# Optimization experiments

Hardware: AMD Instinct MI355X
Metric: run time of the kernel (lower is better)

## Reference

```python
import jax, jax.numpy as jnp
import numpy as np

DIM = 256
B = 8
H = 56
W = 56
K = 2
EPS = 1e-5  # torch BatchNorm2d default eps


def _conv1x1(x, w, b):
    # x: [B,C,H,W], w: [O,C], b: [O]
    return jnp.einsum('oc,bchw->bohw', w, x) + b[None, :, None, None]


def _bn(x, g, be, m, v):
    # inference-mode BatchNorm2d with running stats
    s = g / jnp.sqrt(v + EPS)
    return x * s[None, :, None, None] + (be - m * s)[None, :, None, None]


def _grapher(x, w1, b1, g1, be1, m1, v1, wg, bg, gg, beg, mg, vg, w2, b2, g2, be2, m2, v2):
    # fc1: 1x1 conv + BN
    h = _bn(_conv1x1(x, w1, b1), g1, be1, m1, v1)
    Hh, Ww = h.shape[2], h.shape[3]
    # MRConv4d: running max over circular-shift differences
    # torch.cat([x[:,:,-i:,:], x[:,:,:-i,:]], dim=2) == jnp.roll(x, i, axis=2)
    xj = jnp.zeros_like(h)

    def body_h(c, i):
        return jnp.maximum(c, h - jnp.roll(h, i, axis=2)), None

    xj, _ = jax.lax.scan(body_h, xj, jnp.arange(K, Hh, K))

    def body_w(c, i):
        return jnp.maximum(c, h - jnp.roll(h, i, axis=3)), None

    xj, _ = jax.lax.scan(body_w, xj, jnp.arange(K, Ww, K))

    cat = jnp.concatenate([h, xj], axis=1)  # [B, 2*dim, H, W]
    # MRConv4d.nn: Conv2d(2*dim, 2*dim, 1) -> BN(2*dim) -> GELU (exact erf)
    g = jax.nn.gelu(_bn(_conv1x1(cat, wg, bg), gg, beg, mg, vg), approximate=False)
    # fc2: Conv2d(2*dim, dim, 1) + BN(dim), then residual
    return _bn(_conv1x1(g, w2, b2), g2, be2, m2, v2) + x


def setup_inputs() -> dict:
    key = jax.random.key(0)
    ks = jax.random.split(key, 12)
    d, d2 = DIM, 2 * DIM

    def w(k, o, c):
        return jax.random.normal(k, (o, c), jnp.float32) * np.float32(1.0 / np.sqrt(c))

    return {
        'x': jax.random.normal(ks[0], (B, d, H, W), jnp.float32),
        'w1': w(ks[1], d, d), 'b1': jnp.zeros((d,), jnp.float32),
        'g1': jnp.ones((d,), jnp.float32), 'be1': jnp.zeros((d,), jnp.float32),
        'm1': jax.random.normal(ks[2], (d,), jnp.float32) * 0.1,
        'v1': jax.random.uniform(ks[3], (d,), jnp.float32, 0.5, 1.5),
        'wg': w(ks[4], d2, d2), 'bg': jnp.zeros((d2,), jnp.float32),
        'gg': jnp.ones((d2,), jnp.float32), 'beg': jnp.zeros((d2,), jnp.float32),
        'mg': jax.random.normal(ks[5], (d2,), jnp.float32) * 0.1,
        'vg': jax.random.uniform(ks[6], (d2,), jnp.float32, 0.5, 1.5),
        'w2': w(ks[7], d, d2), 'b2': jnp.zeros((d,), jnp.float32),
        'g2': jnp.ones((d,), jnp.float32), 'be2': jnp.zeros((d,), jnp.float32),
        'm2': jax.random.normal(ks[8], (d,), jnp.float32) * 0.1,
        'v2': jax.random.uniform(ks[9], (d,), jnp.float32, 0.5, 1.5),
    }


def reference(x, w1, b1, g1, be1, m1, v1, wg, bg, gg, beg, mg, vg, w2, b2, g2, be2, m2, v2):
    return _grapher(x, w1, b1, g1, be1, m1, v1, wg, bg, gg, beg, mg, vg, w2, b2, g2, be2, m2, v2)
```

## Files before the change

### kernel.cpp

```cpp
#include <hip/hip_runtime.h>
#include <math.h>

#define SPB 3136
#define NB 8
#define MTOT (NB*SPB)
#define EPS 1e-5f

typedef unsigned short u16;
typedef __attribute__((ext_vector_type(8))) short short8;
typedef __attribute__((ext_vector_type(4))) float float4v;

__device__ __forceinline__ float b2f(u16 v){ unsigned u=((unsigned)v)<<16; float f; __builtin_memcpy(&f,&u,4); return f; }
__device__ __forceinline__ u16 f2b(float f){ unsigned u; __builtin_memcpy(&u,&f,4); u += 0x7fffu + ((u>>16)&1u); return (u16)(u>>16); }
__device__ __forceinline__ float gelu_f(float z){
  float t = 1.5957691216f * z * (1.0f + 0.044715f*z*z);
  return __fdividef(z, 1.0f + __expf(-t));
}

__device__ __forceinline__ void gll16(const u16* g, u16* l){
  __builtin_amdgcn_global_load_lds((const __attribute__((address_space(1))) void*)g,
                                   (__attribute__((address_space(3))) void*)l, 16, 0, 0);
}

__global__ void prep_consts_k(const float* b1,const float* g1,const float* be1,const float* m1,const float* v1,
                              const float* bg,const float* gg,const float* beg,const float* mg,const float* vg,
                              const float* b2,const float* g2,const float* be2,const float* m2,const float* v2,
                              float* cst){
  int i = threadIdx.x;
  if (i < 256) {
    float s = g1[i]*rsqrtf(v1[i]+EPS);
    cst[i] = s; cst[256+i] = b1[i]*s + be1[i] - m1[i]*s;
    float s2 = g2[i]*rsqrtf(v2[i]+EPS);
    cst[1536+i] = s2; cst[1792+i] = b2[i]*s2 + be2[i] - m2[i]*s2;
  }
  float s = gg[i]*rsqrtf(vg[i]+EPS);
  cst[512+i] = s; cst[1024+i] = bg[i]*s + beg[i] - mg[i]*s;
}

__global__ void conv_w_k(const float* __restrict__ w1,const float* __restrict__ wg,const float* __restrict__ w2,
                         u16* __restrict__ w1b,u16* __restrict__ wgb,u16* __restrict__ w2b){
  int i = blockIdx.x*256 + threadIdx.x;
  if (i < 65536)  w1b[i] = f2b(w1[i]);
  if (i < 262144) wgb[i] = f2b(wg[i]);
  if (i < 131072) w2b[i] = f2b(w2[i]);
}

__global__ void transpose_x_k(const float* __restrict__ x, u16* __restrict__ xt){
  __shared__ float t[32][33];
  int b = blockIdx.z, ct = blockIdx.y, st = blockIdx.x;
  int ts = threadIdx.x, tc = threadIdx.y;
  #pragma unroll
  for (int i=0;i<4;i++){
    int c = tc + i*8;
    t[c][ts] = x[((size_t)(b*256 + ct*32 + c))*SPB + st*32 + ts];
  }
  __syncthreads();
  #pragma unroll
  for (int i=0;i<4;i++){
    int r = tc + i*8;
    xt[((size_t)(b*SPB + st*32 + r))*256 + ct*32 + ts] = f2b(t[ts][r]);
  }
}

__global__ void rowmin_k(const u16* __restrict__ cat, float* __restrict__ rmin){
  int b = blockIdx.x/56, y = blockIdx.x%56, c = threadIdx.x;
  float mE=3.4e38f, mO=3.4e38f;
  const u16* base = cat + ((size_t)(b*SPB + y*56))*512 + c;
  for (int x=0;x<56;x+=2){
    mE = fminf(mE, b2f(base[(size_t)x*512]));
    mO = fminf(mO, b2f(base[(size_t)(x+1)*512]));
  }
  rmin[((size_t)(b*2+0)*56 + y)*256 + c]=mE;
  rmin[((size_t)(b*2+1)*56 + y)*256 + c]=mO;
}
__global__ void colmin_k(const u16* __restrict__ cat, float* __restrict__ cmin){
  int b = blockIdx.x/56, x = blockIdx.x%56, c = threadIdx.x;
  float mE=3.4e38f, mO=3.4e38f;
  const u16* base = cat + ((size_t)(b*SPB + x))*512 + c;
  for (int y=0;y<56;y+=2){
    mE = fminf(mE, b2f(base[(size_t)(y*56)*512]));
    mO = fminf(mO, b2f(base[(size_t)((y+1)*56)*512]));
  }
  cmin[((size_t)(b*2+0)*56 + x)*256 + c]=mE;
  cmin[((size_t)(b*2+1)*56 + x)*256 + c]=mO;
}
__global__ void xj_k(u16* __restrict__ cat, const float* __restrict__ rmin, const float* __restrict__ cmin){
  int b = blockIdx.y, s = blockIdx.x, c = threadIdx.x;
  int y = s/56, x = s%56;
  size_t idx = ((size_t)(b*SPB + s))*512;
  float h = b2f(cat[idx + c]);
  float m = fminf(cmin[((size_t)(b*2+(y&1))*56 + x)*256 + c],
                  rmin[((size_t)(b*2+(x&1))*56 + y)*256 + c]);
  cat[idx + 256 + c] = f2b(fmaxf(0.0f, h - m));
}

template<int KTOT, int EPI>
__global__ __launch_bounds__(256) void gemm_k(
    const u16* __restrict__ Ain, const u16* __restrict__ Wt,
    const float* __restrict__ scale, const float* __restrict__ bias,
    void* __restrict__ outp, const float* __restrict__ resid)
{
  __shared__ __align__(16) u16 smem[16896];
  const int tid = threadIdx.x;
  const int m0 = blockIdx.x * 128;
  const int o0 = blockIdx.y * 128;
  const int lane = tid & 63, wid = tid >> 6;
  const int quad = lane >> 4, l16 = lane & 15;
  const int wm = wid & 1, wn = wid >> 1;

  float4v acc[4][4];
  #pragma unroll
  for (int i=0;i<4;i++)
    #pragma unroll
    for (int j=0;j<4;j++) acc[i][j] = (float4v){0.f,0.f,0.f,0.f};

  const int row = tid >> 2, q8 = (tid & 3) * 8;
  const u16* ga0 = Ain + ((size_t)(m0 + row))*KTOT + q8;
  const u16* ga1 = ga0 + (size_t)64*KTOT;
  const u16* gb0 = Wt  + ((size_t)(o0 + row))*KTOT + q8;
  const u16* gb1 = gb0 + (size_t)64*KTOT;
  u16* l8 = smem + tid*8;

  auto STAGE = [&](int kt, int buf){
    u16* b_ = l8 + buf*8192;
    gll16(ga0 + kt, b_);
    gll16(ga1 + kt, b_ + 2048);
    gll16(gb0 + kt, b_ + 4096);
    gll16(gb1 + kt, b_ + 6144);
  };
  auto COMPUTE = [&](int buf){
    const u16* A_ = smem + buf*8192;
    const u16* B_ = A_ + 4096;
    short8 af[4], bfr[4];
    #pragma unroll
    for (int im=0;im<4;im++) af[im]  = *(const short8*)&A_[(wm*64+im*16+l16)*32 + quad*8];
    #pragma unroll
    for (int in=0;in<4;in++) bfr[in] = *(const short8*)&B_[(wn*64+in*16+l16)*32 + quad*8];
    #pragma unroll
    for (int im=0;im<4;im++)
      #pragma unroll
      for (int in=0;in<4;in++)
        acc[im][in] = __builtin_amdgcn_mfma_f32_16x16x32_bf16(af[im], bfr[in], acc[im][in], 0, 0, 0);
  };

  constexpr int NIT = KTOT / 32;
  STAGE(0, 0);
  __syncthreads();
  #pragma unroll
  for (int t = 1; t < NIT; ++t) {
    STAGE(t*32, t & 1);
    COMPUTE((t-1) & 1);
    __syncthreads();
  }
  COMPUTE((NIT-1) & 1);
  __syncthreads();

  if (EPI == 1 || EPI == 2) {
    u16* tile = smem;
    #pragma unroll
    for (int im=0;im<4;im++)
      #pragma unroll
      for (int in=0;in<4;in++){
        int ol = wn*64 + in*16 + l16;
        float sc = scale[o0+ol], bi = bias[o0+ol];
        #pragma unroll
        for (int r=0;r<4;r++){
          float v = acc[im][in][r]*sc + bi;
          if (EPI==2) v = gelu_f(v);
          tile[(wm*64+im*16+quad*4+r)*128 + ol] = f2b(v);
        }
      }
    __syncthreads();
    u16* op = (u16*)outp;
    #pragma unroll
    for (int p=0;p<8;p++){
      int chunk = p*256 + tid;
      int rr = chunk >> 4, off = (chunk & 15)*8;
      *(uint4*)&op[((size_t)(m0 + rr))*512 + o0 + off] = *(const uint4*)&tile[rr*128 + off];
    }
  } else {
    float* ftile = (float*)smem;
    float* op = (float*)outp;
    #pragma unroll
    for (int h=0; h<2; h++){
      if (wn == h){
        #pragma unroll
        for (int im=0;im<4;im++)
          #pragma unroll
          for (int in=0;in<4;in++){
            int c64 = in*16 + l16;
            int og = o0 + h*64 + c64;
            float sc = scale[og], bi = bias[og];
            float4v v;
            #pragma unroll
            for (int r=0;r<4;r++) v[r] = acc[im][in][r]*sc + bi;
            *(float4v*)&ftile[c64*132 + wm*64 + im*16 + quad*4] = v;
          }
      }
      __syncthreads();
      #pragma unroll
      for (int p=0;p<8;p++){
        int chunk = p*256 + tid;
        int rr = chunk >> 5, off = (chunk & 31)*4;
        int m = m0 + off;
        int b = m / SPB, s = m - b*SPB;
        size_t g = ((size_t)(b*256 + o0 + h*64 + rr))*SPB + s;
        float4v v = *(const float4v*)&ftile[rr*132 + off];
        v.x += resid[g]; v.y += resid[g+1]; v.z += resid[g+2]; v.w += resid[g+3];
        *(float4v*)&op[g] = v;
      }
      __syncthreads();
    }
  }
}

extern "C" void kernel_launch(void* const* d_in, const int* in_sizes, int n_in,
                              void* d_out, int out_size, void* d_ws, size_t ws_size,
                              hipStream_t stream)
{
  const float* x  = (const float*)d_in[0];
  const float* w1 = (const float*)d_in[1];
  const float* b1 = (const float*)d_in[2];
  const float* g1 = (const float*)d_in[3];
  const float* be1= (const float*)d_in[4];
  const float* m1 = (const float*)d_in[5];
  const float* v1 = (const float*)d_in[6];
  const float* wg = (const float*)d_in[7];
  const float* bg = (const float*)d_in[8];
  const float* gg = (const float*)d_in[9];
  const float* beg= (const float*)d_in[10];
  const float* mg = (const float*)d_in[11];
  const float* vg = (const float*)d_in[12];
  const float* w2 = (const float*)d_in[13];
  const float* b2 = (const float*)d_in[14];
  const float* g2 = (const float*)d_in[15];
  const float* be2= (const float*)d_in[16];
  const float* m2 = (const float*)d_in[17];
  const float* v2 = (const float*)d_in[18];

  char* ws = (char*)d_ws;
  size_t off = 0;
  auto alloc = [&](size_t bytes){ void* p = ws + off; off += (bytes + 255) & ~(size_t)255; return p; };
  u16* xt    = (u16*)alloc((size_t)MTOT*256*2);
  u16* catt  = (u16*)alloc((size_t)MTOT*512*2);
  u16* gt    = (u16*)alloc((size_t)MTOT*512*2);
  u16* w1b   = (u16*)alloc((size_t)65536*2);
  u16* wgb   = (u16*)alloc((size_t)262144*2);
  u16* w2b   = (u16*)alloc((size_t)131072*2);
  float* cst = (float*)alloc((size_t)2048*4);
  float* rmin= (float*)alloc((size_t)NB*2*56*256*4);
  float* cmin= (float*)alloc((size_t)NB*2*56*256*4);

  hipLaunchKernelGGL(prep_consts_k, dim3(1), dim3(512), 0, stream,
                     b1,g1,be1,m1,v1, bg,gg,beg,mg,vg, b2,g2,be2,m2,v2, cst);
  hipLaunchKernelGGL(conv_w_k, dim3(1024), dim3(256), 0, stream, w1,wg,w2, w1b,wgb,w2b);
  hipLaunchKernelGGL(transpose_x_k, dim3(98,8,8), dim3(32,8), 0, stream, x, xt);
  hipLaunchKernelGGL((gemm_k<256,1>), dim3(196,2), dim3(256), 0, stream,
                     xt, w1b, cst+0, cst+256, (void*)catt, (const float*)nullptr);
  hipLaunchKernelGGL(rowmin_k, dim3(NB*56), dim3(256), 0, stream, catt, rmin);
  hipLaunchKernelGGL(colmin_k, dim3(NB*56), dim3(256), 0, stream, catt, cmin);
  hipLaunchKernelGGL(xj_k, dim3(SPB, NB), dim3(256), 0, stream, catt, rmin, cmin);
  hipLaunchKernelGGL((gemm_k<512,2>), dim3(196,4), dim3(256), 0, stream,
                     catt, wgb, cst+512, cst+1024, (void*)gt, (const float*)nullptr);
  hipLaunchKernelGGL((gemm_k<512,3>), dim3(196,2), dim3(256), 0, stream,
                     gt, w2b, cst+1536, cst+1792, d_out, x);
}
```

Baseline: 195.3 us.

## Triple-buffer GEMM K-loop with explicit waitcnt and vectorize xj kernel

The GEMM main loop moves from double to triple buffering in LDS, prefetching two stages ahead. It replaces __syncthreads with a manual s_waitcnt vmcnt(4) plus s_barrier, so global-to-LDS loads overlap with MFMA compute. Separately, the xj kernel now processes 8 channels per thread with 16-byte vector loads and stores, covering 8 spatial positions per block. The cost is more shared memory per block, which may lower occupancy, and the hand-tuned vmcnt value depends on how many loads STAGE issues.

```diff
diff --git a/kernel.cpp b/kernel.cpp
--- a/kernel.cpp
+++ b/kernel.cpp
@@ -84,14 +84,26 @@
   cmin[((size_t)(b*2+0)*56 + x)*256 + c]=mE;
   cmin[((size_t)(b*2+1)*56 + x)*256 + c]=mO;
 }
-__global__ void xj_k(u16* __restrict__ cat, const float* __restrict__ rmin, const float* __restrict__ cmin){
-  int b = blockIdx.y, s = blockIdx.x, c = threadIdx.x;
+__global__ __launch_bounds__(256) void xj_k(u16* __restrict__ cat, const float* __restrict__ rmin, const float* __restrict__ cmin){
+  int b = blockIdx.y;
+  int t = threadIdx.x;
+  int s = blockIdx.x*8 + (t>>5);
+  int c0 = (t&31)*8;
   int y = s/56, x = s%56;
   size_t idx = ((size_t)(b*SPB + s))*512;
-  float h = b2f(cat[idx + c]);
-  float m = fminf(cmin[((size_t)(b*2+(y&1))*56 + x)*256 + c],
-                  rmin[((size_t)(b*2+(x&1))*56 + y)*256 + c]);
-  cat[idx + 256 + c] = f2b(fmaxf(0.0f, h - m));
+  short8 h8 = *(const short8*)&cat[idx + c0];
+  const float* cp = &cmin[((size_t)(b*2+(y&1))*56 + x)*256 + c0];
+  const float* rp = &rmin[((size_t)(b*2+(x&1))*56 + y)*256 + c0];
+  float4v cv0 = *(const float4v*)cp, cv1 = *(const float4v*)(cp+4);
+  float4v rv0 = *(const float4v*)rp, rv1 = *(const float4v*)(rp+4);
+  short8 o;
+  #pragma unroll
+  for (int j=0;j<8;j++){
+    float cm = (j<4) ? cv0[j] : cv1[j-4];
+    float rm = (j<4) ? rv0[j] : rv1[j-4];
+    o[j] = (short)f2b(fmaxf(0.0f, b2f((u16)h8[j]) - fminf(cm, rm)));
+  }
+  *(short8*)&cat[idx + 256 + c0] = o;
 }
 
 template<int KTOT, int EPI>
@@ -100,7 +112,7 @@
     const float* __restrict__ scale, const float* __restrict__ bias,
     void* __restrict__ outp, const float* __restrict__ resid)
 {
-  __shared__ __align__(16) u16 smem[16896];
+  __shared__ __align__(16) u16 smem[24576];
   const int tid = threadIdx.x;
   const int m0 = blockIdx.x * 128;
   const int o0 = blockIdx.y * 128;
@@ -145,14 +157,17 @@
 
   constexpr int NIT = KTOT / 32;
   STAGE(0, 0);
-  __syncthreads();
-  #pragma unroll
-  for (int t = 1; t < NIT; ++t) {
-    STAGE(t*32, t & 1);
-    COMPUTE((t-1) & 1);
-    __syncthreads();
-  }
-  COMPUTE((NIT-1) & 1);
+  STAGE(32, 1);
+  #pragma unroll
+  for (int t = 0; t < NIT; ++t) {
+    __builtin_amdgcn_sched_barrier(0);
+    if (t + 1 < NIT) asm volatile("s_waitcnt vmcnt(4) lgkmcnt(0)" ::: "memory");
+    else             asm volatile("s_waitcnt vmcnt(0) lgkmcnt(0)" ::: "memory");
+    __builtin_amdgcn_s_barrier();
+    __builtin_amdgcn_sched_barrier(0);
+    if (t + 2 < NIT) STAGE((t+2)*32, (t+2)%3);
+    COMPUTE(t%3);
+  }
   __syncthreads();
 
   if (EPI == 1 || EPI == 2) {
@@ -259,7 +274,7 @@
                      xt, w1b, cst+0, cst+256, (void*)catt, (const float*)nullptr);
   hipLaunchKernelGGL(rowmin_k, dim3(NB*56), dim3(256), 0, stream, catt, rmin);
   hipLaunchKernelGGL(colmin_k, dim3(NB*56), dim3(256), 0, stream, catt, cmin);
-  hipLaunchKernelGGL(xj_k, dim3(SPB, NB), dim3(256), 0, stream, catt, rmin, cmin);
+  hipLaunchKernelGGL(xj_k, dim3(392, NB), dim3(256), 0, stream, catt, rmin, cmin);
   hipLaunchKernelGGL((gemm_k<512,2>), dim3(196,4), dim3(256), 0, stream,
                      catt, wgb, cst+512, cst+1024, (void*)gt, (const float*)nullptr);
   hipLaunchKernelGGL((gemm_k<512,3>), dim3(196,2), dim3(256), 0, stream,
```

New measurement: 186.6 us. -4.4%, faster.
